# Kernel optimization log

Measured on AMD Instinct MI355X. Metric: run time of the kernel, lower is better.

## Reference

```python
import jax, jax.numpy as jnp
import numpy as np

NUM_LAYERS = 6
DIM = 512
VOCAB = 50257
HEADS = 8
EXPERTS = 8
TOPK = 2
LN_EPS = 1e-5


def setup_inputs() -> dict:
    key = jax.random.key(0)
    ks = jax.random.split(key, 9)
    d, L, E = DIM, NUM_LAYERS, EXPERTS
    return {
        'input_ids': jax.random.randint(ks[0], (2, 1024), 0, VOCAB),
        'embed': jax.random.normal(ks[1], (VOCAB, d), dtype=jnp.float32) * 0.02,
        'qkv_w': jax.random.normal(ks[2], (L, 3 * d, d), dtype=jnp.float32) * 0.02,
        'out_w': jax.random.normal(ks[3], (L, d, d), dtype=jnp.float32) * 0.02,
        'router_w': jax.random.normal(ks[4], (L, E, d), dtype=jnp.float32) * 0.02,
        'router_b': jnp.zeros((L, E), dtype=jnp.float32),
        'w1': jax.random.normal(ks[5], (L, E, 2 * d, d), dtype=jnp.float32) * 0.02,
        'b1': jnp.zeros((L, E, 2 * d), dtype=jnp.float32),
        'w2': jax.random.normal(ks[6], (L, E, d, 2 * d), dtype=jnp.float32) * 0.02,
        'b2': jnp.zeros((L, E, d), dtype=jnp.float32),
        'ln_g': jnp.ones((L, d), dtype=jnp.float32),
        'ln_b': jnp.zeros((L, d), dtype=jnp.float32),
        'head_w': jax.random.normal(ks[7], (VOCAB, d), dtype=jnp.float32) * 0.02,
    }


def _bit_weight(w):
    # BitNet 1.58b training-mode effective weight (STE forward value):
    # scale = mean|w| per output row; w_eff = round(w/scale).clip(-1,1) * scale
    scale = jnp.clip(jnp.mean(jnp.abs(w), axis=-1, keepdims=True), 1e-5, None)
    wq = jnp.clip(jnp.round(w / scale), -1.0, 1.0)
    w_ste = jax.lax.stop_gradient(wq - w) + w
    return w_ste * scale


def _layer_norm(x, g, b):
    mu = jnp.mean(x, axis=-1, keepdims=True)
    var = jnp.mean(jnp.square(x - mu), axis=-1, keepdims=True)
    return (x - mu) * jax.lax.rsqrt(var + LN_EPS) * g + b


def _attention(x, qkv_w, out_w):
    B, Lq, D = x.shape
    hd = D // HEADS
    qkv = (x @ qkv_w.T).reshape(B, Lq, 3, HEADS, hd).transpose(2, 0, 3, 1, 4)
    q, k, v = qkv[0], qkv[1], qkv[2]  # [B,H,L,hd]
    attn = jax.nn.softmax(jnp.einsum('bhqd,bhkd->bhqk', q, k) * hd ** -0.5, axis=-1)
    o = jnp.einsum('bhqk,bhkd->bhqd', attn, v).transpose(0, 2, 1, 3).reshape(B, Lq, D)
    return o @ out_w.T


def _moe(x, rw, rb, w1, b1, w2, b2, g, beta):
    B, Lq, D = x.shape
    N = B * Lq
    xf = x.reshape(N, D)
    probs = jax.nn.softmax(xf @ rw.T + rb, axis=-1)  # [N,E]
    vals, idx = jax.lax.top_k(probs, TOPK)
    vals = vals / (jnp.sum(vals, axis=-1, keepdims=True) + 1e-8)
    # combine weights: [N,E] (top-k indices are distinct, so sum == scatter)
    cw = jnp.sum(jax.nn.one_hot(idx, EXPERTS, dtype=xf.dtype) * vals[..., None], axis=1)
    we1 = _bit_weight(w1)  # [E,2D,D]
    we2 = _bit_weight(w2)  # [E,D,2D]
    h = jax.nn.gelu(jnp.einsum('nd,efd->enf', xf, we1) + b1[:, None, :], approximate=False)
    y = jnp.einsum('enf,edf->end', h, we2) + b2[:, None, :]  # [E,N,D]
    out = jnp.einsum('ne,end->nd', cw, y)
    return _layer_norm(out + xf, g, beta).reshape(B, Lq, D)


def reference(input_ids, embed, qkv_w, out_w, router_w, router_b, w1, b1, w2, b2, ln_g, ln_b, head_w):
    x = embed[input_ids]  # [B,L,D]
    for l in range(NUM_LAYERS):
        x = x + _attention(x, qkv_w[l], out_w[l])
        x = _moe(x, router_w[l], router_b[l], w1[l], b1[l], w2[l], b2[l], ln_g[l], ln_b[l])
    return x @ head_w.T  # logits [B,L,V]
```

## Files before the change

kernel.cpp:

```cpp
#include <hip/hip_runtime.h>
#include <math.h>
#include <stdint.h>

#define NLAYER 6
#define DIMD 512
#define HEADS 8
#define HD 64
#define EXPERTS 8
#define SEQ 1024
#define NTOK 2048
#define FF 1024
#define VOCABN 50257
#define HROWS 50432

typedef __bf16 bf16;
typedef __bf16 bf16x8 __attribute__((ext_vector_type(8)));
typedef __bf16 bf16x4 __attribute__((ext_vector_type(4)));
typedef float f32x4 __attribute__((ext_vector_type(4)));

__device__ __forceinline__ void gl_lds16(const void* g, void* l) {
  __builtin_amdgcn_global_load_lds(
      (const __attribute__((address_space(1))) void*)(uintptr_t)g,
      (__attribute__((address_space(3))) void*)(uintptr_t)l, 16, 0, 0);
}

#define LDSW(row, kg) (((row) * 32) + ((((kg) ^ (((row) >> 1) & 3))) << 3))

template <int BNT>
__global__ __launch_bounds__(256) void k_mfma_gemm(
    const bf16* __restrict__ A0, const bf16* __restrict__ A1,
    const bf16* __restrict__ B0, const bf16* __restrict__ B1,
    float* __restrict__ Cf, bf16* __restrict__ Cb0, bf16* __restrict__ Cb1,
    bf16* __restrict__ Cb2, bf16* __restrict__ E0, bf16* __restrict__ E1,
    bf16* __restrict__ E2, int M, int N, int K,
    long sA, long sB, long sCf, long sCb,
    const float* __restrict__ colScale, int csStride,
    const float* __restrict__ bias, int biasStride,
    const float* __restrict__ residual, int act, int mode,
    const int* __restrict__ mLimit, const int* __restrict__ aperm,
    int outmode) {
  constexpr int NI = BNT / 32;
  __shared__ __align__(16) bf16 As[128 * 32];
  __shared__ __align__(16) bf16 Bs[BNT * 32];
  int tid = threadIdx.x;
  int z = blockIdx.z;
  int nwg = gridDim.x * gridDim.y;
  int flat = blockIdx.y * gridDim.x + blockIdx.x;
  int qq = nwg >> 3, rr = nwg & 7;
  int xcd = flat & 7, ii = flat >> 3;
  int swz = (xcd < rr ? xcd * (qq + 1) : rr * (qq + 1) + (xcd - rr) * qq) + ii;
  int m0 = (swz % gridDim.x) * 128, n0 = (swz / gridDim.x) * BNT;
  if (mLimit && m0 >= mLimit[z]) return;
  int w = tid >> 6, lane = tid & 63;
  int wm = (w >> 1) * 64, wn = (w & 1) * (16 * NI);
  int r15 = lane & 15, kg = lane >> 4;

  int pa[3] = {0, 0, 0}, pb[3] = {0, 0, 0};
  int np = 1;
  if (mode == 3) {
    np = 2; pa[1] = 1;
  } else if (mode == 5) {
    np = 3;
    pa[1] = 0; pb[1] = 1; pa[2] = 1; pb[2] = 0;
  }

  f32x4 acc[4][NI] = {};
  int srow = tid >> 2;
  int scol = (((tid & 3) ^ ((tid >> 3) & 3))) << 3;
  long arow0, arow1;
  if (aperm) {
    arow0 = aperm[z * 2048 + m0 + srow];
    arow1 = aperm[z * 2048 + m0 + 64 + srow];
  } else {
    arow0 = m0 + srow;
    arow1 = m0 + 64 + srow;
  }
  const bf16* PA[2] = {A0, A1};
  const bf16* PB[2] = {B0, B1};
  bf16* la0 = &As[tid * 8];
  bf16* la1 = &As[64 * 32 + tid * 8];
  bf16* lb0 = &Bs[tid * 8];

  for (int p = 0; p < np; ++p) {
    const bf16* Az = PA[pa[p]] + (long)z * sA;
    const bf16* Bz = PB[pb[p]] + (long)z * sB;
    const bf16* ga0 = Az + arow0 * K + scol;
    const bf16* ga1 = Az + arow1 * K + scol;
    const bf16* gb0 = Bz + (long)(n0 + srow) * K + scol;
    const bf16* gb1 = (BNT == 128) ? Bz + (long)(n0 + 64 + srow) * K + scol
                                   : nullptr;
    for (int k0 = 0; k0 < K; k0 += 32) {
      gl_lds16(ga0, la0);
      gl_lds16(ga1, la1);
      gl_lds16(gb0, lb0);
      if constexpr (BNT == 128) gl_lds16(gb1, &Bs[64 * 32 + tid * 8]);
      ga0 += 32; ga1 += 32; gb0 += 32;
      if constexpr (BNT == 128) gb1 += 32;
      __syncthreads();
      bf16x8 af[4], bfr[NI];
#pragma unroll
      for (int mi = 0; mi < 4; ++mi) {
        int rowA = wm + mi * 16 + r15;
        af[mi] = *(const bf16x8*)&As[LDSW(rowA, kg)];
      }
#pragma unroll
      for (int ni = 0; ni < NI; ++ni) {
        int rowB = wn + ni * 16 + r15;
        bfr[ni] = *(const bf16x8*)&Bs[LDSW(rowB, kg)];
      }
#pragma unroll
      for (int mi = 0; mi < 4; ++mi)
#pragma unroll
        for (int ni = 0; ni < NI; ++ni)
          acc[mi][ni] = __builtin_amdgcn_mfma_f32_16x16x32_bf16(
              af[mi], bfr[ni], acc[mi][ni], 0, 0, 0);
      __syncthreads();
    }
  }

#pragma unroll
  for (int mi = 0; mi < 4; ++mi) {
    int rbase = m0 + wm + mi * 16 + kg * 4;
#pragma unroll
    for (int ni = 0; ni < NI; ++ni) {
      int col = n0 + wn + ni * 16 + r15;
      if (col >= N) continue;
      float scl = colScale ? colScale[z * csStride + col] : 1.f;
      float bv = bias ? bias[z * biasStride + col] : 0.f;
#pragma unroll
      for (int reg = 0; reg < 4; ++reg) {
        int row = rbase + reg;
        float v = acc[mi][ni][reg] * scl + bv;
        if (act) v = 0.5f * v * (1.f + erff(v * 0.70710678118654752f));
        if (residual) v += residual[(long)row * N + col];
        if (outmode == 2) {
          int b = row >> 10, qt = row & 1023;
          if (n0 < 512) {
            float qv = v * 0.125f;
            int h = col >> 6, d = col & 63;
            long dst = ((long)(b * 8 + h)) * ((long)SEQ * HD) +
                       (long)qt * HD + d;
            bf16 h0 = (bf16)qv;
            Cb0[dst] = h0;
            Cb1[dst] = (bf16)(qv - (float)h0);
          } else if (n0 < 1024) {
            int c2 = col - 512;
            int h = c2 >> 6, d = c2 & 63;
            long dst = ((long)(b * 8 + h)) * ((long)SEQ * HD) +
                       (long)qt * HD + d;
            bf16 h0 = (bf16)v;
            Cb2[dst] = h0;
            E0[dst] = (bf16)(v - (float)h0);
          } else {
            int c2 = col - 1024;
            int h = c2 >> 6, d = c2 & 63;
            long dst = ((long)(b * 8 + h)) * ((long)HD * SEQ) +
                       (long)d * SEQ + qt;
            bf16 h0 = (bf16)v;
            E1[dst] = h0;
            E2[dst] = (bf16)(v - (float)h0);
          }
          continue;
        }
        if (Cf) Cf[z * sCf + (long)row * N + col] = v;
        if (Cb0) {
          long cib = z * sCb + (long)row * N + col;
          bf16 h0 = (bf16)v;
          Cb0[cib] = h0;
          if (Cb1) {
            float r = v - (float)h0;
            Cb1[cib] = (bf16)r;
          }
        }
      }
    }
  }
}

__global__ __launch_bounds__(256) void k_fattn(
    const bf16* __restrict__ q0b, const bf16* __restrict__ q1b,
    const bf16* __restrict__ k0b, const bf16* __restrict__ k1b,
    const bf16* __restrict__ vt0, const bf16* __restrict__ vt1,
    bf16* __restrict__ at0, bf16* __restrict__ at1) {
  __shared__ __align__(16) bf16 Ks[2][128 * 64];
  __shared__ __align__(16) bf16 Vs[2][64 * 128];
  __shared__ __align__(16) bf16 Ps[2][64 * 128];
  int tid = threadIdx.x;
  int bh = blockIdx.y;
  int q0 = blockIdx.x * 64;
  int w = tid >> 6, lane = tid & 63;
  int r15 = lane & 15, kg = lane >> 4;
  const long bhQK = (long)bh * SEQ * HD;
  const long bhV = (long)bh * HD * SEQ;

  bf16x8 qa0[2], qa1[2];
  {
    long qoff = bhQK + (long)(q0 + w * 16 + r15) * HD;
#pragma unroll
    for (int ks = 0; ks < 2; ++ks) {
      qa0[ks] = *(const bf16x8*)&q0b[qoff + ks * 32 + kg * 8];
      qa1[ks] = *(const bf16x8*)&q1b[qoff + ks * 32 + kg * 8];
    }
  }

  auto stageK = [&](int kt) {
#pragma unroll
    for (int i = 0; i < 4; ++i) {
      int L = tid + i * 256;
      int row = L >> 3, pc = L & 7;
      int gc = pc ^ (row & 7);
      long gsrc = bhQK + (long)(kt * 128 + row) * HD + gc * 8;
      gl_lds16(k0b + gsrc, &Ks[0][L * 8]);
      gl_lds16(k1b + gsrc, &Ks[1][L * 8]);
    }
  };
  auto stageV = [&](int kt) {
#pragma unroll
    for (int i = 0; i < 4; ++i) {
      int L = tid + i * 256;
      int row = L >> 4, pc = L & 15;
      int gc = pc ^ (row & 15);
      long gsrc = bhV + (long)row * SEQ + kt * 128 + gc * 8;
      gl_lds16(vt0 + gsrc, &Vs[0][L * 8]);
      gl_lds16(vt1 + gsrc, &Vs[1][L * 8]);
    }
  };
  auto computeS = [&](f32x4* sf) {
#pragma unroll
    for (int kc = 0; kc < 8; ++kc) {
      f32x4 a = {};
      int rowB = kc * 16 + r15;
#pragma unroll
      for (int ks = 0; ks < 2; ++ks) {
        int pc = (ks * 4 + kg) ^ (rowB & 7);
        bf16x8 b0 = *(const bf16x8*)&Ks[0][rowB * 64 + pc * 8];
        bf16x8 b1 = *(const bf16x8*)&Ks[1][rowB * 64 + pc * 8];
        a = __builtin_amdgcn_mfma_f32_16x16x32_bf16(qa0[ks], b0, a, 0, 0, 0);
        a = __builtin_amdgcn_mfma_f32_16x16x32_bf16(qa0[ks], b1, a, 0, 0, 0);
        a = __builtin_amdgcn_mfma_f32_16x16x32_bf16(qa1[ks], b0, a, 0, 0, 0);
      }
      sf[kc] = a;
    }
  };

  float m[4], l[4];
#pragma unroll
  for (int r = 0; r < 4; ++r) { m[r] = -1e30f; l[r] = 0.f; }
  f32x4 oacc[4] = {};

  for (int kt = 0; kt < SEQ / 128; ++kt) {
    stageK(kt);
    stageV(kt);
    __syncthreads();
    f32x4 sf[8];
    computeS(sf);
#pragma unroll
    for (int r = 0; r < 4; ++r) {
      float tm = sf[0][r];
#pragma unroll
      for (int kc = 1; kc < 8; ++kc) tm = fmaxf(tm, sf[kc][r]);
      tm = fmaxf(tm, __shfl_xor(tm, 1));
      tm = fmaxf(tm, __shfl_xor(tm, 2));
      tm = fmaxf(tm, __shfl_xor(tm, 4));
      tm = fmaxf(tm, __shfl_xor(tm, 8));
      float mn = fmaxf(m[r], tm);
      float corr = __expf(m[r] - mn);
      float s = 0.f;
#pragma unroll
      for (int kc = 0; kc < 8; ++kc) {
        float p = __expf(sf[kc][r] - mn);
        sf[kc][r] = p;
        s += p;
      }
      s += __shfl_xor(s, 1);
      s += __shfl_xor(s, 2);
      s += __shfl_xor(s, 4);
      s += __shfl_xor(s, 8);
      l[r] = l[r] * corr + s;
      m[r] = mn;
#pragma unroll
      for (int dg = 0; dg < 4; ++dg) oacc[dg][r] *= corr;
    }
#pragma unroll
    for (int kc = 0; kc < 8; ++kc) {
#pragma unroll
      for (int r = 0; r < 4; ++r) {
        float p = sf[kc][r];
        bf16 h0 = (bf16)p;
        bf16 h1 = (bf16)(p - (float)h0);
        int qrow = w * 16 + kg * 4 + r;
        int kcol = kc * 16 + r15;
        int pc = (kcol >> 3) ^ (qrow & 15);
        int addr = qrow * 128 + pc * 8 + (kcol & 7);
        Ps[0][addr] = h0;
        Ps[1][addr] = h1;
      }
    }
    bf16x8 pa0[4], pa1[4];
    int rowP = w * 16 + r15;
#pragma unroll
    for (int ks = 0; ks < 4; ++ks) {
      int pc = (ks * 4 + kg) ^ (rowP & 15);
      pa0[ks] = *(const bf16x8*)&Ps[0][rowP * 128 + pc * 8];
      pa1[ks] = *(const bf16x8*)&Ps[1][rowP * 128 + pc * 8];
    }
#pragma unroll
    for (int dg = 0; dg < 4; ++dg) {
      int rowV = dg * 16 + r15;
#pragma unroll
      for (int ks = 0; ks < 4; ++ks) {
        int pc = (ks * 4 + kg) ^ (rowV & 15);
        bf16x8 v0 = *(const bf16x8*)&Vs[0][rowV * 128 + pc * 8];
        bf16x8 v1 = *(const bf16x8*)&Vs[1][rowV * 128 + pc * 8];
        oacc[dg] = __builtin_amdgcn_mfma_f32_16x16x32_bf16(pa0[ks], v0,
                                                           oacc[dg], 0, 0, 0);
        oacc[dg] = __builtin_amdgcn_mfma_f32_16x16x32_bf16(pa0[ks], v1,
                                                           oacc[dg], 0, 0, 0);
        oacc[dg] = __builtin_amdgcn_mfma_f32_16x16x32_bf16(pa1[ks], v0,
                                                           oacc[dg], 0, 0, 0);
      }
    }
    __syncthreads();
  }

  float invl[4];
#pragma unroll
  for (int r = 0; r < 4; ++r) invl[r] = 1.f / l[r];

  int b = bh >> 3, h = bh & 7;
#pragma unroll
  for (int dg = 0; dg < 4; ++dg) {
#pragma unroll
    for (int r = 0; r < 4; ++r) {
      int qrow = q0 + w * 16 + kg * 4 + r;
      int d = dg * 16 + r15;
      long dst = ((long)(b * SEQ + qrow)) * DIMD + h * HD + d;
      float v = oacc[dg][r] * invl[r];
      bf16 h0 = (bf16)v;
      at0[dst] = h0;
      at1[dst] = (bf16)(v - (float)h0);
    }
  }
}

__global__ __launch_bounds__(512, 2) void k_hgemm(const bf16* __restrict__ A,
                                                  const bf16* __restrict__ Bt,
                                                  float* __restrict__ C,
                                                  int M, int N, int K) {
  __shared__ __align__(16) bf16 As[2][256 * 64];
  __shared__ __align__(16) bf16 Bs[2][256 * 64];
  int tid = threadIdx.x;
  int nwg = gridDim.x * gridDim.y;
  int flat = blockIdx.y * gridDim.x + blockIdx.x;
  int qq = nwg >> 3, rr = nwg & 7;
  int xcd = flat & 7, ii = flat >> 3;
  int swz = (xcd < rr ? xcd * (qq + 1) : rr * (qq + 1) + (xcd - rr) * qq) + ii;
  int m0 = (swz % gridDim.x) * 256, n0 = (swz / gridDim.x) * 256;
  int w = tid >> 6, lane = tid & 63;
  int wm = (w >> 2) * 128, wn = (w & 3) * 64;
  int r15 = lane & 15, kg = lane >> 4;

  auto stage = [&](int buf, int kt) {
#pragma unroll
    for (int j = 0; j < 4; ++j) {
      int L = tid + j * 512;
      int row = L >> 3, pc = L & 7;
      int gc = pc ^ (row & 7);
      gl_lds16(A + (long)(m0 + row) * K + kt * 64 + gc * 8, &As[buf][L * 8]);
      gl_lds16(Bt + (long)(n0 + row) * K + kt * 64 + gc * 8, &Bs[buf][L * 8]);
    }
  };

  f32x4 acc[8][4] = {};
  auto compute = [&](int buf) {
#pragma unroll
    for (int ks = 0; ks < 2; ++ks) {
      bf16x8 af[8], bf_[4];
#pragma unroll
      for (int mi = 0; mi < 8; ++mi) {
        int row = wm + mi * 16 + r15;
        af[mi] = *(const bf16x8*)
            &As[buf][row * 64 + ((((ks * 4 + kg) ^ (row & 7))) << 3)];
      }
#pragma unroll
      for (int ni = 0; ni < 4; ++ni) {
        int row = wn + ni * 16 + r15;
        bf_[ni] = *(const bf16x8*)
            &Bs[buf][row * 64 + ((((ks * 4 + kg) ^ (row & 7))) << 3)];
      }
#pragma unroll
      for (int mi = 0; mi < 8; ++mi)
#pragma unroll
        for (int ni = 0; ni < 4; ++ni)
          acc[mi][ni] = __builtin_amdgcn_mfma_f32_16x16x32_bf16(
              af[mi], bf_[ni], acc[mi][ni], 0, 0, 0);
    }
  };

  stage(0, 0);
  stage(1, 1);
#pragma unroll 1
  for (int t = 0; t < 6; ++t) {
    asm volatile("s_waitcnt vmcnt(8)" ::: "memory");
    __builtin_amdgcn_s_barrier();
    __builtin_amdgcn_sched_barrier(0);
    compute(t & 1);
    __builtin_amdgcn_s_barrier();
    stage(t & 1, t + 2);
  }
  asm volatile("s_waitcnt vmcnt(8)" ::: "memory");
  __builtin_amdgcn_s_barrier();
  __builtin_amdgcn_sched_barrier(0);
  compute(0);
  asm volatile("s_waitcnt vmcnt(0)" ::: "memory");
  __builtin_amdgcn_s_barrier();
  __builtin_amdgcn_sched_barrier(0);
  compute(1);

#pragma unroll
  for (int mi = 0; mi < 8; ++mi) {
    int rbase = m0 + wm + mi * 16 + kg * 4;
#pragma unroll
    for (int ni = 0; ni < 4; ++ni) {
      int col = n0 + wn + ni * 16 + r15;
      if (col >= N) continue;
#pragma unroll
      for (int reg = 0; reg < 4; ++reg)
        C[(long)(rbase + reg) * N + col] = acc[mi][ni][reg];
    }
  }
}

__global__ __launch_bounds__(256) void k_embed(const int* __restrict__ ids,
                                               const float* __restrict__ E,
                                               float* __restrict__ xf,
                                               bf16* __restrict__ x0,
                                               bf16* __restrict__ x1) {
  int i = blockIdx.x * 256 + threadIdx.x;
  if (i >= NTOK * DIMD) return;
  int n = i >> 9, d = i & 511;
  float v = E[(long)ids[n] * DIMD + d];
  xf[i] = v;
  bf16 b0 = (bf16)v;
  x0[i] = b0;
  x1[i] = (bf16)(v - (float)b0);
}

__global__ __launch_bounds__(256) void k_prepw(const float* __restrict__ qkv_w,
                                               const float* __restrict__ out_w,
                                               bf16* __restrict__ qw0a,
                                               bf16* __restrict__ qw1a,
                                               bf16* __restrict__ ow0a,
                                               bf16* __restrict__ ow1a) {
  int l = blockIdx.y;
  const long n8q = (long)3 * DIMD * DIMD / 8;
  long i = (long)blockIdx.x * 256 + threadIdx.x;
  const float* s;
  bf16 *d0, *d1;
  long j;
  if (i < n8q) {
    s = qkv_w + (long)l * 3 * DIMD * DIMD;
    d0 = qw0a + (long)l * 3 * DIMD * DIMD;
    d1 = qw1a + (long)l * 3 * DIMD * DIMD;
    j = i;
  } else {
    s = out_w + (long)l * DIMD * DIMD;
    d0 = ow0a + (long)l * DIMD * DIMD;
    d1 = ow1a + (long)l * DIMD * DIMD;
    j = i - n8q;
  }
  const float4* s4 = (const float4*)s;
  float4 a = s4[2 * j], b = s4[2 * j + 1];
  float vv[8] = {a.x, a.y, a.z, a.w, b.x, b.y, b.z, b.w};
  bf16x8 o0, o1;
#pragma unroll
  for (int k = 0; k < 8; ++k) {
    float v = vv[k];
    bf16 h0 = (bf16)v;
    o0[k] = h0;
    o1[k] = (bf16)(v - (float)h0);
  }
  ((bf16x8*)d0)[j] = o0;
  ((bf16x8*)d1)[j] = o1;
}

__global__ __launch_bounds__(256) void k_headconv(const float* __restrict__ s,
                                                  bf16* __restrict__ d) {
  long i = (long)blockIdx.x * 256 + threadIdx.x;
  long n8 = (long)HROWS * DIMD / 8;
  if (i >= n8) return;
  long row = i / (DIMD / 8);
  bf16x8 o;
  if (row < VOCABN) {
    const float4* s4 = (const float4*)s;
    float4 a = s4[2 * i], b = s4[2 * i + 1];
    o[0] = (bf16)a.x; o[1] = (bf16)a.y; o[2] = (bf16)a.z; o[3] = (bf16)a.w;
    o[4] = (bf16)b.x; o[5] = (bf16)b.y; o[6] = (bf16)b.z; o[7] = (bf16)b.w;
  } else {
    o = (bf16x8)(bf16)0.f;
  }
  ((bf16x8*)d)[i] = o;
}

__global__ __launch_bounds__(64) void k_router(const float* __restrict__ x,
                                               const float* __restrict__ rw,
                                               const float* __restrict__ rb,
                                               int* __restrict__ top2,
                                               float* __restrict__ v2) {
  int n = blockIdx.x;
  int t = threadIdx.x;
  int e = t >> 3, part = t & 7;
  __shared__ float red[64];
  const float* xr = x + (long)n * DIMD;
  const float* wr = rw + (long)e * DIMD;
  float d = 0.f;
  int c0 = part * 64;
#pragma unroll
  for (int c = 0; c < 64; c += 4) {
    float4 xv = *(const float4*)(xr + c0 + c);
    float4 wv = *(const float4*)(wr + c0 + c);
    d += xv.x * wv.x + xv.y * wv.y + xv.z * wv.z + xv.w * wv.w;
  }
  red[t] = d;
  __syncthreads();
  if (t < 8) {
    float logit = rb[t];
    for (int pp = 0; pp < 8; ++pp) logit += red[t * 8 + pp];
    red[t] = logit;
  }
  __syncthreads();
  if (t == 0) {
    float p2[8];
    float m = -1e30f;
    for (int i = 0; i < 8; ++i) m = fmaxf(m, red[i]);
    float s = 0.f;
    for (int i = 0; i < 8; ++i) { p2[i] = expf(red[i] - m); s += p2[i]; }
    for (int i = 0; i < 8; ++i) p2[i] /= s;
    int i1 = 0;
    for (int i = 1; i < 8; ++i) if (p2[i] > p2[i1]) i1 = i;
    int i2 = (i1 == 0) ? 1 : 0;
    for (int i = 0; i < 8; ++i) {
      if (i == i1 || i == i2) continue;
      if (p2[i] > p2[i2]) i2 = i;
    }
    float sum = p2[i1] + p2[i2] + 1e-8f;
    top2[2 * n] = i1;
    top2[2 * n + 1] = i2;
    v2[2 * n] = p2[i1] / sum;
    v2[2 * n + 1] = p2[i2] / sum;
  }
}

__global__ __launch_bounds__(256) void k_expcnt(const int* __restrict__ top2,
                                                int* __restrict__ perm,
                                                int* __restrict__ tokpos,
                                                int* __restrict__ cnt,
                                                bf16* __restrict__ zx0,
                                                bf16* __restrict__ zx1) {
  int e = blockIdx.x, t = threadIdx.x;
  if (e == 0) {
    for (int c = t; c < DIMD; c += 256) {
      zx0[c] = (bf16)0.f;
      zx1[c] = (bf16)0.f;
    }
  }
  __shared__ int sc[256];
  int fl[8];
  int f = 0;
#pragma unroll
  for (int j = 0; j < 8; ++j) {
    int n = t * 8 + j;
    int m = (top2[2 * n] == e || top2[2 * n + 1] == e) ? 1 : 0;
    fl[j] = m;
    f += m;
  }
  sc[t] = f;
  __syncthreads();
  for (int o = 1; o < 256; o <<= 1) {
    int v = (t >= o) ? sc[t - o] : 0;
    __syncthreads();
    sc[t] += v;
    __syncthreads();
  }
  int pos = sc[t] - f;
#pragma unroll
  for (int j = 0; j < 8; ++j) {
    if (fl[j]) {
      int n = t * 8 + j;
      perm[e * 2048 + pos] = n;
      int jj = (top2[2 * n] == e) ? 0 : 1;
      tokpos[2 * n + jj] = e * 2048 + pos;
      ++pos;
    }
  }
  int total = sc[255];
  int cpad = (total + 127) & ~127;
  for (int i = total + t; i < cpad; i += 256) perm[e * 2048 + i] = 2048;
  if (t == 0) cnt[e] = total;
}

__global__ __launch_bounds__(256) void k_bitw2(const float* __restrict__ w1,
                                               const float* __restrict__ w2,
                                               bf16* __restrict__ we1qa,
                                               float* __restrict__ s1a,
                                               bf16* __restrict__ we2qa,
                                               float* __restrict__ s2a) {
  int l = blockIdx.y;
  int blk = blockIdx.x;
  int t = threadIdx.x;
  const float* wr;
  bf16* outr;
  float* sOut;
  int cols;
  if (blk < EXPERTS * FF) {
    cols = DIMD;
    wr = w1 + (long)l * EXPERTS * FF * DIMD + (long)blk * cols;
    outr = we1qa + (long)l * EXPERTS * FF * DIMD + (long)blk * cols;
    sOut = s1a + (long)l * EXPERTS * FF + blk;
  } else {
    int row = blk - EXPERTS * FF;
    cols = FF;
    wr = w2 + (long)l * EXPERTS * DIMD * FF + (long)row * cols;
    outr = we2qa + (long)l * EXPERTS * DIMD * FF + (long)row * cols;
    sOut = s2a + (long)l * EXPERTS * DIMD + row;
  }
  float acc = 0.f;
  for (int c = t; c < cols; c += 256) acc += fabsf(wr[c]);
  __shared__ float red[256];
  red[t] = acc;
  __syncthreads();
  for (int off = 128; off; off >>= 1) {
    if (t < off) red[t] += red[t + off];
    __syncthreads();
  }
  float scale = fmaxf(red[0] / (float)cols, 1e-5f);
  if (t == 0) *sOut = scale;
  for (int c = t; c < cols; c += 256) {
    float qv = rintf(wr[c] / scale);
    qv = fmaxf(-1.f, fminf(1.f, qv));
    outr[c] = (bf16)qv;
  }
}

__global__ __launch_bounds__(128) void k_lncomb(
    const float* __restrict__ yg, const int* __restrict__ tokpos,
    const float* __restrict__ v2, const float* __restrict__ xBf,
    const float* __restrict__ g, const float* __restrict__ b,
    float* __restrict__ xof, bf16* __restrict__ x0, bf16* __restrict__ x1) {
  int n = blockIdx.x;
  int t = threadIdx.x;
  __shared__ float red[128];
  long tp0 = tokpos[2 * n], tp1 = tokpos[2 * n + 1];
  float w0 = v2[2 * n], w1 = v2[2 * n + 1];
  const float* y0 = yg + tp0 * DIMD;
  const float* y1 = yg + tp1 * DIMD;
  float u[4];
  float s = 0.f;
#pragma unroll
  for (int i = 0; i < 4; ++i) {
    int d = t + i * 128;
    float v = xBf[(long)n * DIMD + d] + w0 * y0[d] + w1 * y1[d];
    u[i] = v;
    s += v;
  }
  red[t] = s;
  __syncthreads();
  for (int off = 64; off; off >>= 1) {
    if (t < off) red[t] += red[t + off];
    __syncthreads();
  }
  float mu = red[0] / (float)DIMD;
  __syncthreads();
  float var = 0.f;
#pragma unroll
  for (int i = 0; i < 4; ++i) {
    float d = u[i] - mu;
    var += d * d;
  }
  red[t] = var;
  __syncthreads();
  for (int off = 64; off; off >>= 1) {
    if (t < off) red[t] += red[t + off];
    __syncthreads();
  }
  float inv = 1.f / sqrtf(red[0] / (float)DIMD + 1e-5f);
#pragma unroll
  for (int i = 0; i < 4; ++i) {
    int c = t + i * 128;
    float v = (u[i] - mu) * inv * g[c] + b[c];
    long oi = (long)n * DIMD + c;
    xof[oi] = v;
    bf16 b0 = (bf16)v;
    x0[oi] = b0;
    x1[oi] = (bf16)(v - (float)b0);
  }
}

extern "C" void kernel_launch(void* const* d_in, const int* in_sizes, int n_in,
                              void* d_out, int out_size, void* d_ws, size_t ws_size,
                              hipStream_t stream) {
  const int* ids = (const int*)d_in[0];
  const float* embed = (const float*)d_in[1];
  const float* qkv_w = (const float*)d_in[2];
  const float* out_w = (const float*)d_in[3];
  const float* router_w = (const float*)d_in[4];
  const float* router_b = (const float*)d_in[5];
  const float* w1 = (const float*)d_in[6];
  const float* b1 = (const float*)d_in[7];
  const float* w2 = (const float*)d_in[8];
  const float* b2 = (const float*)d_in[9];
  const float* ln_g = (const float*)d_in[10];
  const float* ln_b = (const float*)d_in[11];
  const float* head_w = (const float*)d_in[12];
  float* out = (float*)d_out;

  char* base = (char*)d_ws;
  size_t off = 0;
  auto alloc = [&](size_t bytes) -> void* {
    void* p = base + off;
    off += (bytes + 255) & ~(size_t)255;
    return p;
  };
  const size_t ND = (size_t)NTOK * DIMD;
  float* xAf = (float*)alloc(ND * 4);
  float* xBf = (float*)alloc(ND * 4);
  int* top2 = (int*)alloc((size_t)NTOK * 2 * 4);
  float* v2 = (float*)alloc((size_t)NTOK * 2 * 4);
  int* perm = (int*)alloc((size_t)EXPERTS * 2048 * 4);
  int* tokpos = (int*)alloc((size_t)NTOK * 2 * 4);
  int* cntb = (int*)alloc(64);
  bf16* xA0 = (bf16*)alloc(ND * 2);
  bf16* xA1 = (bf16*)alloc(ND * 2);
  bf16* xB0 = (bf16*)alloc((ND + DIMD) * 2);
  bf16* xB1 = (bf16*)alloc((ND + DIMD) * 2);
  bf16* at0 = (bf16*)alloc(ND * 2);
  bf16* at1 = (bf16*)alloc(ND * 2);
  bf16* q0b = (bf16*)alloc((size_t)16 * SEQ * HD * 2);
  bf16* q1b = (bf16*)alloc((size_t)16 * SEQ * HD * 2);
  bf16* k0b = (bf16*)alloc((size_t)16 * SEQ * HD * 2);
  bf16* k1b = (bf16*)alloc((size_t)16 * SEQ * HD * 2);
  bf16* vt0b = (bf16*)alloc((size_t)16 * HD * SEQ * 2);
  bf16* vt1b = (bf16*)alloc((size_t)16 * HD * SEQ * 2);
  bf16* qw0a = (bf16*)alloc((size_t)NLAYER * 3 * DIMD * DIMD * 2);
  bf16* qw1a = (bf16*)alloc((size_t)NLAYER * 3 * DIMD * DIMD * 2);
  bf16* ow0a = (bf16*)alloc((size_t)NLAYER * DIMD * DIMD * 2);
  bf16* ow1a = (bf16*)alloc((size_t)NLAYER * DIMD * DIMD * 2);
  bf16* we1qa = (bf16*)alloc((size_t)NLAYER * EXPERTS * FF * DIMD * 2);
  float* s1a = (float*)alloc((size_t)NLAYER * EXPERTS * FF * 4);
  bf16* we2qa = (bf16*)alloc((size_t)NLAYER * EXPERTS * DIMD * FF * 2);
  float* s2a = (float*)alloc((size_t)NLAYER * EXPERTS * DIMD * 4);

  size_t Ustart = off;
  bf16* h0g = (bf16*)alloc((size_t)EXPERTS * 2048 * FF * 2);
  bf16* h1g = (bf16*)alloc((size_t)EXPERTS * 2048 * FF * 2);
  float* yg = (float*)alloc((size_t)EXPERTS * 2048 * DIMD * 4);
  size_t endB = off;
  size_t endC = Ustart + (size_t)HROWS * DIMD * 2;
  bf16* hw0 = (bf16*)(base + Ustart);
  off = endB > endC ? endB : endC;
  if (ws_size < off) return;

  k_embed<<<(NTOK * DIMD + 255) / 256, 256, 0, stream>>>(ids, embed, xAf, xA0,
                                                         xA1);
  k_prepw<<<dim3(512, NLAYER), 256, 0, stream>>>(qkv_w, out_w, qw0a, qw1a,
                                                 ow0a, ow1a);
  k_bitw2<<<dim3(EXPERTS * FF + EXPERTS * DIMD, NLAYER), 256, 0, stream>>>(
      w1, w2, we1qa, s1a, we2qa, s2a);

  for (int l = 0; l < NLAYER; ++l) {
    bf16* qw0 = qw0a + (long)l * 3 * DIMD * DIMD;
    bf16* qw1 = qw1a + (long)l * 3 * DIMD * DIMD;
    bf16* ow0 = ow0a + (long)l * DIMD * DIMD;
    bf16* ow1 = ow1a + (long)l * DIMD * DIMD;
    bf16* we1q = we1qa + (long)l * EXPERTS * FF * DIMD;
    bf16* we2q = we2qa + (long)l * EXPERTS * DIMD * FF;
    float* s1 = s1a + (long)l * EXPERTS * FF;
    float* s2 = s2a + (long)l * EXPERTS * DIMD;
    k_mfma_gemm<128><<<dim3(NTOK / 128, (3 * DIMD) / 128, 1), 256, 0,
                       stream>>>(
        xA0, xA1, qw0, qw1, nullptr, q0b, q1b, k0b, k1b, vt0b, vt1b,
        NTOK, 3 * DIMD, DIMD, 0, 0, 0, 0,
        nullptr, 0, nullptr, 0, nullptr, 0, 5, nullptr, nullptr, 2);
    k_fattn<<<dim3(SEQ / 64, 16), 256, 0, stream>>>(q0b, q1b, k0b, k1b,
                                                    vt0b, vt1b, at0, at1);
    k_mfma_gemm<128><<<dim3(NTOK / 128, DIMD / 128, 1), 256, 0, stream>>>(
        at0, at1, ow0, ow1, xBf, xB0, xB1, nullptr, nullptr, nullptr,
        nullptr, NTOK, DIMD, DIMD, 0, 0, 0, 0,
        nullptr, 0, nullptr, 0, xAf, 0, 5, nullptr, nullptr, 0);
    k_router<<<NTOK, 64, 0, stream>>>(xBf, router_w + (long)l * EXPERTS * DIMD,
                                      router_b + l * EXPERTS, top2, v2);
    k_expcnt<<<EXPERTS, 256, 0, stream>>>(top2, perm, tokpos, cntb,
                                          xB0 + ND, xB1 + ND);
    k_mfma_gemm<128><<<dim3(NTOK / 128, FF / 128, EXPERTS), 256, 0, stream>>>(
        xB0, xB1, we1q, nullptr, nullptr, h0g, h1g, nullptr, nullptr, nullptr,
        nullptr, NTOK, FF, DIMD, 0, (long)FF * DIMD, 0, (long)2048 * FF,
        s1, FF, b1 + (long)l * EXPERTS * FF, FF, nullptr, 1, 3, cntb, perm, 0);
    k_mfma_gemm<128><<<dim3(NTOK / 128, DIMD / 128, EXPERTS), 256, 0,
                       stream>>>(
        h0g, h1g, we2q, nullptr, yg, nullptr, nullptr, nullptr, nullptr,
        nullptr, nullptr, NTOK, DIMD, FF, (long)2048 * FF, (long)DIMD * FF,
        (long)2048 * DIMD, 0, s2, DIMD, b2 + (long)l * EXPERTS * DIMD, DIMD,
        nullptr, 0, 3, cntb, nullptr, 0);
    k_lncomb<<<NTOK, 128, 0, stream>>>(yg, tokpos, v2, xBf, ln_g + l * DIMD,
                                       ln_b + l * DIMD, xAf, xA0, xA1);
  }
  long nh8 = (long)HROWS * DIMD / 8;
  k_headconv<<<(int)((nh8 + 255) / 256), 256, 0, stream>>>(head_w, hw0);
  k_hgemm<<<dim3(NTOK / 256, HROWS / 256, 1), 512, 0, stream>>>(
      xA0, hw0, out, NTOK, VOCABN, DIMD);
}
```

Measured before the change: 2.257 ms.

## Double-buffer LDS tiles in the MFMA GEMM with a two-stage prefetch pipeline

The GEMM kernel now keeps two LDS buffers for the A and B tiles and flattens the multi-pass K loop into one pipelined loop. Global-to-LDS loads for the next tiles are issued while the current tile is computed, using explicit vmcnt waits and barriers in place of two full syncs per iteration. The goal is to hide global load latency behind MFMA work. It doubles LDS use per block, which may lower occupancy, and drops the unused BNT template parameter.

```diff
diff --git a/kernel.cpp b/kernel.cpp
--- a/kernel.cpp
+++ b/kernel.cpp
@@ -26,7 +26,6 @@
 
 #define LDSW(row, kg) (((row) * 32) + ((((kg) ^ (((row) >> 1) & 3))) << 3))
 
-template <int BNT>
 __global__ __launch_bounds__(256) void k_mfma_gemm(
     const bf16* __restrict__ A0, const bf16* __restrict__ A1,
     const bf16* __restrict__ B0, const bf16* __restrict__ B1,
@@ -39,9 +38,8 @@
     const float* __restrict__ residual, int act, int mode,
     const int* __restrict__ mLimit, const int* __restrict__ aperm,
     int outmode) {
-  constexpr int NI = BNT / 32;
-  __shared__ __align__(16) bf16 As[128 * 32];
-  __shared__ __align__(16) bf16 Bs[BNT * 32];
+  __shared__ __align__(16) bf16 As[2][128 * 32];
+  __shared__ __align__(16) bf16 Bs[2][128 * 32];
   int tid = threadIdx.x;
   int z = blockIdx.z;
   int nwg = gridDim.x * gridDim.y;
@@ -49,10 +47,10 @@
   int qq = nwg >> 3, rr = nwg & 7;
   int xcd = flat & 7, ii = flat >> 3;
   int swz = (xcd < rr ? xcd * (qq + 1) : rr * (qq + 1) + (xcd - rr) * qq) + ii;
-  int m0 = (swz % gridDim.x) * 128, n0 = (swz / gridDim.x) * BNT;
+  int m0 = (swz % gridDim.x) * 128, n0 = (swz / gridDim.x) * 128;
   if (mLimit && m0 >= mLimit[z]) return;
   int w = tid >> 6, lane = tid & 63;
-  int wm = (w >> 1) * 64, wn = (w & 1) * (16 * NI);
+  int wm = (w >> 1) * 64, wn = (w & 1) * 64;
   int r15 = lane & 15, kg = lane >> 4;
 
   int pa[3] = {0, 0, 0}, pb[3] = {0, 0, 0};
@@ -64,7 +62,7 @@
     pa[1] = 0; pb[1] = 1; pa[2] = 1; pb[2] = 0;
   }
 
-  f32x4 acc[4][NI] = {};
+  f32x4 acc[4][4] = {};
   int srow = tid >> 2;
   int scol = (((tid & 3) ^ ((tid >> 3) & 3))) << 3;
   long arow0, arow1;
@@ -77,52 +75,76 @@
   }
   const bf16* PA[2] = {A0, A1};
   const bf16* PB[2] = {B0, B1};
-  bf16* la0 = &As[tid * 8];
-  bf16* la1 = &As[64 * 32 + tid * 8];
-  bf16* lb0 = &Bs[tid * 8];
-
-  for (int p = 0; p < np; ++p) {
+
+  const int kIters = K / 32;
+  const int nIter = np * kIters;
+  int sp = 0, staged = 0;
+  const bf16 *sa0, *sa1, *sb0, *sb1;
+  auto resetPassPtrs = [&](int p) {
     const bf16* Az = PA[pa[p]] + (long)z * sA;
     const bf16* Bz = PB[pb[p]] + (long)z * sB;
-    const bf16* ga0 = Az + arow0 * K + scol;
-    const bf16* ga1 = Az + arow1 * K + scol;
-    const bf16* gb0 = Bz + (long)(n0 + srow) * K + scol;
-    const bf16* gb1 = (BNT == 128) ? Bz + (long)(n0 + 64 + srow) * K + scol
-                                   : nullptr;
-    for (int k0 = 0; k0 < K; k0 += 32) {
-      gl_lds16(ga0, la0);
-      gl_lds16(ga1, la1);
-      gl_lds16(gb0, lb0);
-      if constexpr (BNT == 128) gl_lds16(gb1, &Bs[64 * 32 + tid * 8]);
-      ga0 += 32; ga1 += 32; gb0 += 32;
-      if constexpr (BNT == 128) gb1 += 32;
-      __syncthreads();
-      bf16x8 af[4], bfr[NI];
-#pragma unroll
-      for (int mi = 0; mi < 4; ++mi) {
-        int rowA = wm + mi * 16 + r15;
-        af[mi] = *(const bf16x8*)&As[LDSW(rowA, kg)];
-      }
-#pragma unroll
-      for (int ni = 0; ni < NI; ++ni) {
-        int rowB = wn + ni * 16 + r15;
-        bfr[ni] = *(const bf16x8*)&Bs[LDSW(rowB, kg)];
-      }
-#pragma unroll
-      for (int mi = 0; mi < 4; ++mi)
-#pragma unroll
-        for (int ni = 0; ni < NI; ++ni)
-          acc[mi][ni] = __builtin_amdgcn_mfma_f32_16x16x32_bf16(
-              af[mi], bfr[ni], acc[mi][ni], 0, 0, 0);
-      __syncthreads();
-    }
-  }
+    sa0 = Az + arow0 * K + scol;
+    sa1 = Az + arow1 * K + scol;
+    sb0 = Bz + (long)(n0 + srow) * K + scol;
+    sb1 = Bz + (long)(n0 + 64 + srow) * K + scol;
+  };
+  resetPassPtrs(0);
+  auto stage = [&](int buf) {
+    gl_lds16(sa0, &As[buf][tid * 8]);
+    gl_lds16(sa1, &As[buf][2048 + tid * 8]);
+    gl_lds16(sb0, &Bs[buf][tid * 8]);
+    gl_lds16(sb1, &Bs[buf][2048 + tid * 8]);
+    sa0 += 32; sa1 += 32; sb0 += 32; sb1 += 32;
+    if (++staged == kIters) {
+      staged = 0;
+      if (++sp < np) resetPassPtrs(sp);
+    }
+  };
+  auto compute = [&](int buf) {
+    bf16x8 af[4], bfr[4];
+#pragma unroll
+    for (int mi = 0; mi < 4; ++mi) {
+      int rowA = wm + mi * 16 + r15;
+      af[mi] = *(const bf16x8*)&As[buf][LDSW(rowA, kg)];
+    }
+#pragma unroll
+    for (int ni = 0; ni < 4; ++ni) {
+      int rowB = wn + ni * 16 + r15;
+      bfr[ni] = *(const bf16x8*)&Bs[buf][LDSW(rowB, kg)];
+    }
+#pragma unroll
+    for (int mi = 0; mi < 4; ++mi)
+#pragma unroll
+      for (int ni = 0; ni < 4; ++ni)
+        acc[mi][ni] = __builtin_amdgcn_mfma_f32_16x16x32_bf16(
+            af[mi], bfr[ni], acc[mi][ni], 0, 0, 0);
+  };
+
+  stage(0);
+  stage(1);
+#pragma unroll 1
+  for (int it = 0; it < nIter - 2; ++it) {
+    asm volatile("s_waitcnt vmcnt(4)" ::: "memory");
+    __builtin_amdgcn_s_barrier();
+    __builtin_amdgcn_sched_barrier(0);
+    compute(it & 1);
+    __builtin_amdgcn_s_barrier();
+    stage(it & 1);
+  }
+  asm volatile("s_waitcnt vmcnt(4)" ::: "memory");
+  __builtin_amdgcn_s_barrier();
+  __builtin_amdgcn_sched_barrier(0);
+  compute(nIter & 1);
+  asm volatile("s_waitcnt vmcnt(0)" ::: "memory");
+  __builtin_amdgcn_s_barrier();
+  __builtin_amdgcn_sched_barrier(0);
+  compute((nIter - 1) & 1);
 
 #pragma unroll
   for (int mi = 0; mi < 4; ++mi) {
     int rbase = m0 + wm + mi * 16 + kg * 4;
 #pragma unroll
-    for (int ni = 0; ni < NI; ++ni) {
+    for (int ni = 0; ni < 4; ++ni) {
       int col = n0 + wn + ni * 16 + r15;
       if (col >= N) continue;
       float scl = colScale ? colScale[z * csStride + col] : 1.f;
@@ -776,14 +798,13 @@
     bf16* we2q = we2qa + (long)l * EXPERTS * DIMD * FF;
     float* s1 = s1a + (long)l * EXPERTS * FF;
     float* s2 = s2a + (long)l * EXPERTS * DIMD;
-    k_mfma_gemm<128><<<dim3(NTOK / 128, (3 * DIMD) / 128, 1), 256, 0,
-                       stream>>>(
+    k_mfma_gemm<<<dim3(NTOK / 128, (3 * DIMD) / 128, 1), 256, 0, stream>>>(
         xA0, xA1, qw0, qw1, nullptr, q0b, q1b, k0b, k1b, vt0b, vt1b,
         NTOK, 3 * DIMD, DIMD, 0, 0, 0, 0,
         nullptr, 0, nullptr, 0, nullptr, 0, 5, nullptr, nullptr, 2);
     k_fattn<<<dim3(SEQ / 64, 16), 256, 0, stream>>>(q0b, q1b, k0b, k1b,
                                                     vt0b, vt1b, at0, at1);
-    k_mfma_gemm<128><<<dim3(NTOK / 128, DIMD / 128, 1), 256, 0, stream>>>(
+    k_mfma_gemm<<<dim3(NTOK / 128, DIMD / 128, 1), 256, 0, stream>>>(
         at0, at1, ow0, ow1, xBf, xB0, xB1, nullptr, nullptr, nullptr,
         nullptr, NTOK, DIMD, DIMD, 0, 0, 0, 0,
         nullptr, 0, nullptr, 0, xAf, 0, 5, nullptr, nullptr, 0);
@@ -791,12 +812,11 @@
                                       router_b + l * EXPERTS, top2, v2);
     k_expcnt<<<EXPERTS, 256, 0, stream>>>(top2, perm, tokpos, cntb,
                                           xB0 + ND, xB1 + ND);
-    k_mfma_gemm<128><<<dim3(NTOK / 128, FF / 128, EXPERTS), 256, 0, stream>>>(
+    k_mfma_gemm<<<dim3(NTOK / 128, FF / 128, EXPERTS), 256, 0, stream>>>(
         xB0, xB1, we1q, nullptr, nullptr, h0g, h1g, nullptr, nullptr, nullptr,
         nullptr, NTOK, FF, DIMD, 0, (long)FF * DIMD, 0, (long)2048 * FF,
         s1, FF, b1 + (long)l * EXPERTS * FF, FF, nullptr, 1, 3, cntb, perm, 0);
-    k_mfma_gemm<128><<<dim3(NTOK / 128, DIMD / 128, EXPERTS), 256, 0,
-                       stream>>>(
+    k_mfma_gemm<<<dim3(NTOK / 128, DIMD / 128, EXPERTS), 256, 0, stream>>>(
         h0g, h1g, we2q, nullptr, yg, nullptr, nullptr, nullptr, nullptr,
         nullptr, nullptr, NTOK, DIMD, FF, (long)2048 * FF, (long)DIMD * FF,
         (long)2048 * DIMD, 0, s2, DIMD, b2 + (long)l * EXPERTS * DIMD, DIMD,
```

Result: faster. 2.058 ms (-8.8%).
